# Kernel tuning notes

Hardware: AMD Instinct MI355X
Metric: run time of the kernel (lower is better)

The kernel has to match this reference:

```python
import math
import jax, jax.numpy as jnp
import numpy as np

EMBED = 1024
INTERNAL = 1024  # EMBED // downsample_rate(=1)
HEADS = 16


def setup_inputs() -> dict:
    key = jax.random.key(0)
    ks = jax.random.split(key, 11)
    b, n, m = 2, 2048, 2048
    s = 1.0 / math.sqrt(EMBED)
    inp = {
        "q": jax.random.normal(ks[0], (b, n, EMBED), jnp.float32),
        "k": jax.random.normal(ks[1], (b, m, EMBED), jnp.float32),
        "v": jax.random.normal(ks[2], (b, m, EMBED), jnp.float32),
        # Linear params (torch Linear: y = x @ W.T + b); store as [in, out].
        "Wq": jax.random.normal(ks[3], (EMBED, INTERNAL), jnp.float32) * s,
        "bq": jax.random.normal(ks[4], (INTERNAL,), jnp.float32) * s,
        "Wk": jax.random.normal(ks[5], (EMBED, INTERNAL), jnp.float32) * s,
        "bk": jax.random.normal(ks[6], (INTERNAL,), jnp.float32) * s,
        "Wv": jax.random.normal(ks[7], (EMBED, INTERNAL), jnp.float32) * s,
        "bv": jax.random.normal(ks[8], (INTERNAL,), jnp.float32) * s,
        "Wo": jax.random.normal(ks[9], (INTERNAL, EMBED), jnp.float32) * s,
        "bo": jax.random.normal(ks[10], (EMBED,), jnp.float32) * s,
    }
    return inp


def _split_heads(x):  # [b, n, c] -> [b, h, n, c/h]
    b, n, c = x.shape
    return x.reshape(b, n, HEADS, c // HEADS).transpose(0, 2, 1, 3)


def reference(q, k, v, Wq, bq, Wk, bk, Wv, bv, Wo, bo):
    qh = _split_heads(q @ Wq + bq)
    kh = _split_heads(k @ Wk + bk)
    vh = _split_heads(v @ Wv + bv)
    c_per_head = kh.shape[-1]
    attn = jnp.einsum("bhnc,bhmc->bhnm", qh, kh) / math.sqrt(c_per_head)
    attn = jax.nn.softmax(attn, axis=-1)
    out = jnp.einsum("bhnm,bhmc->bhnc", attn, vh)
    b, h, n, ch = out.shape
    out = out.transpose(0, 2, 1, 3).reshape(b, n, h * ch)
    return out @ Wo + bo
```

## Files before the change

kernel.cpp:

```cpp
#include <hip/hip_runtime.h>

#define EMBED 1024
#define HEADS 16
#define DHEAD 64
#define BATCH 2
#define SEQ 2048
#define ROWS (BATCH*SEQ)
#define SZA (ROWS*EMBED)
#define SW (EMBED*EMBED)

typedef _Float16 f16;
typedef __attribute__((ext_vector_type(2))) __fp16 h16x2;
typedef __attribute__((ext_vector_type(4))) _Float16 f16x4;
typedef __attribute__((ext_vector_type(8))) _Float16 f16x8;
typedef __attribute__((ext_vector_type(4))) float f32x4;

__device__ __forceinline__ void gld16(const f16* g, f16* lds) {
  __builtin_amdgcn_global_load_lds(
      (const __attribute__((address_space(1))) void*)g,
      (__attribute__((address_space(3))) void*)lds, 16, 0, 0);
}

__global__ __launch_bounds__(256) void pre_kernel(
    const float* __restrict__ q, const float* __restrict__ k,
    const float* __restrict__ v, f16* __restrict__ qc,
    f16* __restrict__ kc, f16* __restrict__ vc,
    const float* __restrict__ w0, const float* __restrict__ w1,
    const float* __restrict__ w2, const float* __restrict__ w3,
    f16* __restrict__ o0, f16* __restrict__ o1,
    f16* __restrict__ o2, f16* __restrict__ o3) {
  __shared__ float tile[32][33];
  const int y = blockIdx.y;
  if (y < 3) {
    const float* in = y == 0 ? q : y == 1 ? k : v;
    f16* out       = y == 0 ? qc : y == 1 ? kc : vc;
    int i = blockIdx.x * 256 + threadIdx.x;
    float4 f = ((const float4* __restrict__)in)[i];
    union { f16 h[4]; short4 s4; } u;
    u.h[0] = (f16)f.x; u.h[1] = (f16)f.y; u.h[2] = (f16)f.z; u.h[3] = (f16)f.w;
    ((short4* __restrict__)out)[i] = u.s4;
    return;
  }
  const int x = blockIdx.x;
  const int z = x >> 10, by = (x >> 5) & 31, bx = x & 31;
  const float* in = z == 0 ? w0 : z == 1 ? w1 : z == 2 ? w2 : w3;
  f16* out       = z == 0 ? o0 : z == 1 ? o1 : z == 2 ? o2 : o3;
  int tx = threadIdx.x & 31, ty = threadIdx.x >> 5;
  #pragma unroll
  for (int i = 0; i < 32; i += 8)
    tile[ty + i][tx] = in[(by*32 + ty + i)*EMBED + bx*32 + tx];
  __syncthreads();
  #pragma unroll
  for (int i = 0; i < 32; i += 8)
    out[(bx*32 + ty + i)*EMBED + by*32 + tx] = (f16)tile[tx][ty + i];
}

__global__ __launch_bounds__(256) void gemm3_kernel(
    const f16* __restrict__ qc, const f16* __restrict__ kc, const f16* __restrict__ vc,
    const f16* __restrict__ Wqt, const f16* __restrict__ Wkt, const f16* __restrict__ Wvt,
    const float* __restrict__ bq, const float* __restrict__ bk, const float* __restrict__ bv,
    f16* __restrict__ Qp, f16* __restrict__ Kp, f16* __restrict__ Vtg) {
  __shared__ __align__(16) f16 As[128*32];
  __shared__ __align__(16) f16 Bs[128*32];
  const int z = blockIdx.y;
  const f16 *A, *Bt; const float* bias; f16* C;
  int mbase, nbase, N, biasrow;
  if (z == 0)      { A=qc;  Bt=Wqt; bias=bq; C=Qp;  mbase=(blockIdx.x&31)*128; nbase=(blockIdx.x>>5)*128; N=EMBED; biasrow=0; }
  else if (z == 1) { A=kc;  Bt=Wkt; bias=bk; C=Kp;  mbase=(blockIdx.x&31)*128; nbase=(blockIdx.x>>5)*128; N=EMBED; biasrow=0; }
  else             { A=Wvt; Bt=vc;  bias=bv; C=Vtg; mbase=(blockIdx.x&7)*128;  nbase=(blockIdx.x>>3)*128; N=ROWS;  biasrow=1; }
  const int K = EMBED;
  const int tid = threadIdx.x;
  const int wave = tid >> 6, lane = tid & 63;
  const int lg = lane >> 4, lr = lane & 15;
  const int wm = (wave >> 1) * 64, wn = (wave & 1) * 64;
  const int sr = lane >> 2, sc = (lane & 3) * 8;
  const f16* gA0 = A  + (size_t)(mbase + wave*16 + sr)*K + sc;
  const f16* gA1 = A  + (size_t)(mbase + 64 + wave*16 + sr)*K + sc;
  const f16* gB0 = Bt + (size_t)(nbase + wave*16 + sr)*K + sc;
  const f16* gB1 = Bt + (size_t)(nbase + 64 + wave*16 + sr)*K + sc;
  f16* lA0 = &As[(wave*16)*32];
  f16* lA1 = &As[(64 + wave*16)*32];
  f16* lB0 = &Bs[(wave*16)*32];
  f16* lB1 = &Bs[(64 + wave*16)*32];
  f32x4 acc[4][4] = {};
  for (int k0 = 0; k0 < K; k0 += 32) {
    __syncthreads();
    gld16(gA0 + k0, lA0);
    gld16(gA1 + k0, lA1);
    gld16(gB0 + k0, lB0);
    gld16(gB1 + k0, lB1);
    __syncthreads();
    f16x8 af[4], bf[4];
    #pragma unroll
    for (int mt = 0; mt < 4; mt++)
      af[mt] = *(const f16x8*)&As[(wm + mt*16 + lr)*32 + lg*8];
    #pragma unroll
    for (int nt = 0; nt < 4; nt++)
      bf[nt] = *(const f16x8*)&Bs[(wn + nt*16 + lr)*32 + lg*8];
    #pragma unroll
    for (int mt = 0; mt < 4; mt++)
      #pragma unroll
      for (int nt = 0; nt < 4; nt++)
        acc[mt][nt] = __builtin_amdgcn_mfma_f32_16x16x32_f16(af[mt], bf[nt], acc[mt][nt], 0, 0, 0);
  }
  #pragma unroll
  for (int mt = 0; mt < 4; mt++)
    #pragma unroll
    for (int nt = 0; nt < 4; nt++)
      #pragma unroll
      for (int i = 0; i < 4; i++) {
        int row = mbase + wm + mt*16 + lg*4 + i;
        int col = nbase + wn + nt*16 + lr;
        float val = acc[mt][nt][i] + (biasrow ? bias[row] : bias[col]);
        if (z == 0) val *= 0.18033688011f;
        C[(size_t)row*N + col] = (f16)val;
      }
}

__global__ __launch_bounds__(256) void gemmo_kernel(
    const f16* __restrict__ A, const f16* __restrict__ Bt,
    const float* __restrict__ bias, float* __restrict__ Cf) {
  __shared__ __align__(16) f16 As[128*32];
  __shared__ __align__(16) f16 Bs[64*32];
  const int K = EMBED, N = EMBED;
  const int tid = threadIdx.x;
  const int wave = tid >> 6, lane = tid & 63;
  const int lg = lane >> 4, lr = lane & 15;
  const int mbase = blockIdx.x * 128, nbase = blockIdx.y * 64;
  const int wm = (wave >> 1) * 64, wn = (wave & 1) * 32;
  const int sr = wave*16 + (lane >> 2), sc = (lane & 3) * 8;
  const f16* gA0 = A  + (size_t)(mbase + sr)*K + sc;
  const f16* gA1 = A  + (size_t)(mbase + 64 + sr)*K + sc;
  const f16* gB  = Bt + (size_t)(nbase + sr)*K + sc;
  f16* lA0 = &As[(wave*16)*32];
  f16* lA1 = &As[(64 + wave*16)*32];
  f16* lB  = &Bs[(wave*16)*32];
  f32x4 acc[4][2] = {};
  for (int k0 = 0; k0 < K; k0 += 32) {
    __syncthreads();
    gld16(gA0 + k0, lA0);
    gld16(gA1 + k0, lA1);
    gld16(gB  + k0, lB);
    __syncthreads();
    f16x8 af[4], bf[2];
    #pragma unroll
    for (int mt = 0; mt < 4; mt++)
      af[mt] = *(const f16x8*)&As[(wm + mt*16 + lr)*32 + lg*8];
    #pragma unroll
    for (int nt = 0; nt < 2; nt++)
      bf[nt] = *(const f16x8*)&Bs[(wn + nt*16 + lr)*32 + lg*8];
    #pragma unroll
    for (int mt = 0; mt < 4; mt++)
      #pragma unroll
      for (int nt = 0; nt < 2; nt++)
        acc[mt][nt] = __builtin_amdgcn_mfma_f32_16x16x32_f16(af[mt], bf[nt], acc[mt][nt], 0, 0, 0);
  }
  #pragma unroll
  for (int mt = 0; mt < 4; mt++)
    #pragma unroll
    for (int nt = 0; nt < 2; nt++)
      #pragma unroll
      for (int i = 0; i < 4; i++) {
        int row = mbase + wm + mt*16 + lg*4 + i;
        int col = nbase + wn + nt*16 + lr;
        Cf[(size_t)row*N + col] = acc[mt][nt][i] + bias[col];
      }
}

__global__ __launch_bounds__(256, 2) void attn_kernel(
    const f16* __restrict__ Qp, const f16* __restrict__ Kp,
    const f16* __restrict__ Vt, f16* __restrict__ Ob) {
  __shared__ __align__(16) f16 Ks[2*4096];
  __shared__ __align__(16) f16 Vs[2*4096];
  const int tid = threadIdx.x;
  const int wave = tid >> 6, lane = tid & 63;
  const int lg = lane >> 4, lr = lane & 15;
  const int gid = blockIdx.x;
  const int bh  = (gid & 7)*4 + ((gid >> 3) & 3);
  const int qblk = gid >> 5;
  const int h = bh & 15, b = bh >> 4;
  const int q0 = qblk*128 + wave*32;
  const f16* Qh = Qp + (size_t)b*SEQ*EMBED + h*DHEAD;
  const f16* Kh = Kp + (size_t)b*SEQ*EMBED + h*DHEAD;
  const f16* Vh = Vt + (size_t)h*DHEAD*ROWS + (size_t)b*SEQ;

  const f16* kst[2]; const f16* vst[2]; f16* kdst[2]; f16* vdst[2];
  #pragma unroll
  for (int m = 0; m < 2; m++) {
    int sgrp = m*4 + wave;
    int srow = sgrp*8 + (lane >> 3);
    int sch  = (lane & 7) ^ (srow & 7);
    int prow = ((srow>>5)&1)*32 + ((srow>>4)&1)*4 + ((srow>>2)&3)*8 + (srow&3);
    kst[m] = Kh + (size_t)prow*EMBED + sch*8;
    vst[m] = Vh + (size_t)srow*ROWS + sch*8;
    kdst[m] = &Ks[sgrp*512];
    vdst[m] = &Vs[sgrp*512];
  }

  f16x8 qf[2][2];
  #pragma unroll
  for (int qb = 0; qb < 2; qb++)
    #pragma unroll
    for (int ds = 0; ds < 2; ds++)
      qf[qb][ds] = *(const f16x8*)&Qh[(size_t)(q0 + qb*16 + lr)*EMBED + ds*32 + lg*8];

  const int c0 = ((lg)     ^ (lr & 7)) * 8;
  const int c1 = ((4 + lg) ^ (lr & 7)) * 8;

  f32x4 o[4][2] = {};
  f32x4 lacc[2] = {};
  const f32x4 NEG8 = {-8.f, -8.f, -8.f, -8.f};
  f16x8 onesf;
  #pragma unroll
  for (int i = 0; i < 8; i++) onesf[i] = (f16)1.0f;

  gld16(kst[0], kdst[0]);
  gld16(kst[1], kdst[1]);
  gld16(vst[0], vdst[0]);
  gld16(vst[1], vdst[1]);
  __syncthreads();

  #pragma unroll 2
  for (int t = 0; t < 32; ++t) {
    const int bo = (t & 1) * 4096;
    if (t < 31) {
      const int po = 4096 - bo;
      const size_t kt = (size_t)(t + 1) * 64;
      gld16(kst[0] + kt*EMBED, kdst[0] + po);
      gld16(kst[1] + kt*EMBED, kdst[1] + po);
      gld16(vst[0] + kt, vdst[0] + po);
      gld16(vst[1] + kt, vdst[1] + po);
    }

    f16x8 ka[4][2];
    #pragma unroll
    for (int nb = 0; nb < 4; nb++) {
      ka[nb][0] = *(const f16x8*)&Ks[bo + (nb*16 + lr)*64 + c0];
      ka[nb][1] = *(const f16x8*)&Ks[bo + (nb*16 + lr)*64 + c1];
    }
    f32x4 sa[2][4];
    __builtin_amdgcn_s_setprio(1);
    #pragma unroll
    for (int nb = 0; nb < 4; nb++)
      #pragma unroll
      for (int qb = 0; qb < 2; qb++) {
        f32x4 z = __builtin_amdgcn_mfma_f32_16x16x32_f16(ka[nb][0], qf[qb][0], NEG8, 0, 0, 0);
        sa[qb][nb] = __builtin_amdgcn_mfma_f32_16x16x32_f16(ka[nb][1], qf[qb][1], z, 0, 0, 0);
      }
    __builtin_amdgcn_s_setprio(0);

    f16x8 va[4][2];
    #pragma unroll
    for (int dm = 0; dm < 4; dm++) {
      va[dm][0] = *(const f16x8*)&Vs[bo + (dm*16 + lr)*64 + c0];
      va[dm][1] = *(const f16x8*)&Vs[bo + (dm*16 + lr)*64 + c1];
    }

    f16x8 pf[2][2];
    #pragma unroll
    for (int qb = 0; qb < 2; qb++) {
      float p[4][4];
      #pragma unroll
      for (int nb = 0; nb < 4; nb++)
        #pragma unroll
        for (int i = 0; i < 4; i++)
          p[nb][i] = __builtin_amdgcn_exp2f(sa[qb][nb][i]);
      union { f16x8 v; h16x2 h2[4]; } u0, u1;
      u0.h2[0] = __builtin_amdgcn_cvt_pkrtz(p[0][0], p[0][1]);
      u0.h2[1] = __builtin_amdgcn_cvt_pkrtz(p[0][2], p[0][3]);
      u0.h2[2] = __builtin_amdgcn_cvt_pkrtz(p[1][0], p[1][1]);
      u0.h2[3] = __builtin_amdgcn_cvt_pkrtz(p[1][2], p[1][3]);
      u1.h2[0] = __builtin_amdgcn_cvt_pkrtz(p[2][0], p[2][1]);
      u1.h2[1] = __builtin_amdgcn_cvt_pkrtz(p[2][2], p[2][3]);
      u1.h2[2] = __builtin_amdgcn_cvt_pkrtz(p[3][0], p[3][1]);
      u1.h2[3] = __builtin_amdgcn_cvt_pkrtz(p[3][2], p[3][3]);
      pf[qb][0] = u0.v;
      pf[qb][1] = u1.v;
    }

    __builtin_amdgcn_s_setprio(1);
    #pragma unroll
    for (int ks = 0; ks < 2; ks++)
      #pragma unroll
      for (int qb = 0; qb < 2; qb++) {
        #pragma unroll
        for (int dm = 0; dm < 4; dm++)
          o[dm][qb] = __builtin_amdgcn_mfma_f32_16x16x32_f16(va[dm][ks], pf[qb][ks], o[dm][qb], 0, 0, 0);
        lacc[qb] = __builtin_amdgcn_mfma_f32_16x16x32_f16(onesf, pf[qb][ks], lacc[qb], 0, 0, 0);
      }
    __builtin_amdgcn_s_setprio(0);

    __syncthreads();
  }

  const float inv[2] = { 1.f / lacc[0][0], 1.f / lacc[1][0] };

  #pragma unroll
  for (int qb = 0; qb < 2; qb++) {
    const size_t rowb = (size_t)(b*SEQ + q0 + qb*16 + lr)*EMBED + h*DHEAD;
    #pragma unroll
    for (int dm = 0; dm < 4; dm++) {
      f16x4 w;
      #pragma unroll
      for (int i = 0; i < 4; i++) w[i] = (f16)(o[dm][qb][i] * inv[qb]);
      *(f16x4*)&Ob[rowb + dm*16 + 4*lg] = w;
    }
  }
}

extern "C" void kernel_launch(void* const* d_in, const int* in_sizes, int n_in,
                              void* d_out, int out_size, void* d_ws, size_t ws_size,
                              hipStream_t stream) {
  (void)in_sizes; (void)n_in; (void)out_size; (void)ws_size;
  const float* q  = (const float*)d_in[0];
  const float* k  = (const float*)d_in[1];
  const float* v  = (const float*)d_in[2];
  const float* Wq = (const float*)d_in[3];
  const float* bq = (const float*)d_in[4];
  const float* Wk = (const float*)d_in[5];
  const float* bk = (const float*)d_in[6];
  const float* Wv = (const float*)d_in[7];
  const float* bv = (const float*)d_in[8];
  const float* Wo = (const float*)d_in[9];
  const float* bo = (const float*)d_in[10];
  float* out = (float*)d_out;

  f16* w   = (f16*)d_ws;
  f16* qc  = w;
  f16* kc  = qc + SZA;
  f16* vc  = kc + SZA;
  f16* Qp  = vc + SZA;
  f16* Kp  = Qp + SZA;
  f16* Vtg = Kp + SZA;
  f16* Ob  = Vtg + SZA;
  f16* Wqt = Ob + SZA;
  f16* Wkt = Wqt + SW;
  f16* Wvt = Wkt + SW;
  f16* Wot = Wvt + SW;

  dim3 pg(4096, 4);
  pre_kernel<<<pg, 256, 0, stream>>>(q, k, v, qc, kc, vc,
                                     Wq, Wk, Wv, Wo, Wqt, Wkt, Wvt, Wot);
  dim3 g3(256, 3);
  gemm3_kernel<<<g3, 256, 0, stream>>>(qc, kc, vc, Wqt, Wkt, Wvt, bq, bk, bv, Qp, Kp, Vtg);
  attn_kernel<<<512, 256, 0, stream>>>(Qp, Kp, Vtg, Ob);
  dim3 go(ROWS/128, EMBED/64);
  gemmo_kernel<<<go, 256, 0, stream>>>(Ob, Wot, bo, out);
}
```

Measured before the change: 207.1 us.

## Double-buffer LDS and XOR-swizzle tiles in projection GEMM kernels

```diff
diff --git a/kernel.cpp b/kernel.cpp
--- a/kernel.cpp
+++ b/kernel.cpp
@@ -60,8 +60,8 @@
     const f16* __restrict__ Wqt, const f16* __restrict__ Wkt, const f16* __restrict__ Wvt,
     const float* __restrict__ bq, const float* __restrict__ bk, const float* __restrict__ bv,
     f16* __restrict__ Qp, f16* __restrict__ Kp, f16* __restrict__ Vtg) {
-  __shared__ __align__(16) f16 As[128*32];
-  __shared__ __align__(16) f16 Bs[128*32];
+  __shared__ __align__(16) f16 As[2*4096];
+  __shared__ __align__(16) f16 Bs[2*4096];
   const int z = blockIdx.y;
   const f16 *A, *Bt; const float* bias; f16* C;
   int mbase, nbase, N, biasrow;
@@ -73,7 +73,8 @@
   const int wave = tid >> 6, lane = tid & 63;
   const int lg = lane >> 4, lr = lane & 15;
   const int wm = (wave >> 1) * 64, wn = (wave & 1) * 64;
-  const int sr = lane >> 2, sc = (lane & 3) * 8;
+  const int sr = lane >> 2;
+  const int sc = ((lane & 3) ^ ((lane >> 3) & 3)) * 8;
   const f16* gA0 = A  + (size_t)(mbase + wave*16 + sr)*K + sc;
   const f16* gA1 = A  + (size_t)(mbase + 64 + wave*16 + sr)*K + sc;
   const f16* gB0 = Bt + (size_t)(nbase + wave*16 + sr)*K + sc;
@@ -82,26 +83,39 @@
   f16* lA1 = &As[(64 + wave*16)*32];
   f16* lB0 = &Bs[(wave*16)*32];
   f16* lB1 = &Bs[(64 + wave*16)*32];
+  const int csw = (lg ^ ((lr >> 1) & 3)) * 8;
   f32x4 acc[4][4] = {};
-  for (int k0 = 0; k0 < K; k0 += 32) {
-    __syncthreads();
-    gld16(gA0 + k0, lA0);
-    gld16(gA1 + k0, lA1);
-    gld16(gB0 + k0, lB0);
-    gld16(gB1 + k0, lB1);
-    __syncthreads();
+
+  gld16(gA0, lA0);
+  gld16(gA1, lA1);
+  gld16(gB0, lB0);
+  gld16(gB1, lB1);
+  __syncthreads();
+
+  #pragma unroll 2
+  for (int t = 0; t < 32; ++t) {
+    const int bo = (t & 1) * 4096;
+    if (t < 31) {
+      const int po = 4096 - bo;
+      const int k0 = (t + 1) * 32;
+      gld16(gA0 + k0, lA0 + po);
+      gld16(gA1 + k0, lA1 + po);
+      gld16(gB0 + k0, lB0 + po);
+      gld16(gB1 + k0, lB1 + po);
+    }
     f16x8 af[4], bf[4];
     #pragma unroll
     for (int mt = 0; mt < 4; mt++)
-      af[mt] = *(const f16x8*)&As[(wm + mt*16 + lr)*32 + lg*8];
+      af[mt] = *(const f16x8*)&As[bo + (wm + mt*16 + lr)*32 + csw];
     #pragma unroll
     for (int nt = 0; nt < 4; nt++)
-      bf[nt] = *(const f16x8*)&Bs[(wn + nt*16 + lr)*32 + lg*8];
+      bf[nt] = *(const f16x8*)&Bs[bo + (wn + nt*16 + lr)*32 + csw];
     #pragma unroll
     for (int mt = 0; mt < 4; mt++)
       #pragma unroll
       for (int nt = 0; nt < 4; nt++)
         acc[mt][nt] = __builtin_amdgcn_mfma_f32_16x16x32_f16(af[mt], bf[nt], acc[mt][nt], 0, 0, 0);
+    __syncthreads();
   }
   #pragma unroll
   for (int mt = 0; mt < 4; mt++)
@@ -120,40 +134,52 @@
 __global__ __launch_bounds__(256) void gemmo_kernel(
     const f16* __restrict__ A, const f16* __restrict__ Bt,
     const float* __restrict__ bias, float* __restrict__ Cf) {
-  __shared__ __align__(16) f16 As[128*32];
-  __shared__ __align__(16) f16 Bs[64*32];
+  __shared__ __align__(16) f16 As[2*4096];
+  __shared__ __align__(16) f16 Bs[2*2048];
   const int K = EMBED, N = EMBED;
   const int tid = threadIdx.x;
   const int wave = tid >> 6, lane = tid & 63;
   const int lg = lane >> 4, lr = lane & 15;
   const int mbase = blockIdx.x * 128, nbase = blockIdx.y * 64;
   const int wm = (wave >> 1) * 64, wn = (wave & 1) * 32;
-  const int sr = wave*16 + (lane >> 2), sc = (lane & 3) * 8;
+  const int sr = wave*16 + (lane >> 2);
+  const int sc = ((lane & 3) ^ ((lane >> 3) & 3)) * 8;
   const f16* gA0 = A  + (size_t)(mbase + sr)*K + sc;
   const f16* gA1 = A  + (size_t)(mbase + 64 + sr)*K + sc;
   const f16* gB  = Bt + (size_t)(nbase + sr)*K + sc;
   f16* lA0 = &As[(wave*16)*32];
   f16* lA1 = &As[(64 + wave*16)*32];
   f16* lB  = &Bs[(wave*16)*32];
+  const int csw = (lg ^ ((lr >> 1) & 3)) * 8;
   f32x4 acc[4][2] = {};
-  for (int k0 = 0; k0 < K; k0 += 32) {
-    __syncthreads();
-    gld16(gA0 + k0, lA0);
-    gld16(gA1 + k0, lA1);
-    gld16(gB  + k0, lB);
-    __syncthreads();
+
+  gld16(gA0, lA0);
+  gld16(gA1, lA1);
+  gld16(gB,  lB);
+  __syncthreads();
+
+  #pragma unroll 2
+  for (int t = 0; t < 32; ++t) {
+    const int boA = (t & 1) * 4096, boB = (t & 1) * 2048;
+    if (t < 31) {
+      const int k0 = (t + 1) * 32;
+      gld16(gA0 + k0, lA0 + (4096 - boA));
+      gld16(gA1 + k0, lA1 + (4096 - boA));
+      gld16(gB  + k0, lB  + (2048 - boB));
+    }
     f16x8 af[4], bf[2];
     #pragma unroll
     for (int mt = 0; mt < 4; mt++)
-      af[mt] = *(const f16x8*)&As[(wm + mt*16 + lr)*32 + lg*8];
+      af[mt] = *(const f16x8*)&As[boA + (wm + mt*16 + lr)*32 + csw];
     #pragma unroll
     for (int nt = 0; nt < 2; nt++)
-      bf[nt] = *(const f16x8*)&Bs[(wn + nt*16 + lr)*32 + lg*8];
+      bf[nt] = *(const f16x8*)&Bs[boB + (wn + nt*16 + lr)*32 + csw];
     #pragma unroll
     for (int mt = 0; mt < 4; mt++)
       #pragma unroll
       for (int nt = 0; nt < 2; nt++)
         acc[mt][nt] = __builtin_amdgcn_mfma_f32_16x16x32_f16(af[mt], bf[nt], acc[mt][nt], 0, 0, 0);
+    __syncthreads();
   }
   #pragma unroll
   for (int mt = 0; mt < 4; mt++)
```

After: 224.0 us. 1.08x slower.
